# Performance work log

Hardware: AMD Instinct MI355X
Metric: run time of the kernel (lower is better)

Reference implementation:

```python
import jax, jax.numpy as jnp
import numpy as np

THRESHOLD = 0.004  # graph_threshold from init_kwargs
EPS = 1e-12


def setup_inputs() -> dict:
    key = jax.random.key(0)
    kf, kw = jax.random.split(key)
    features = jax.random.normal(kf, (8192, 128), dtype=jnp.float32)
    weight = jax.random.normal(kw, (128, 128), dtype=jnp.float32)
    return {"features": features, "weight": weight}


def reference(features, weight):
    # Pairwise state fidelity: squared dot product of row-normalized vectors.
    n = features.shape[0]
    xn = features / (jnp.linalg.norm(features, axis=1, keepdims=True) + EPS)
    fid = (xn @ xn.T) ** 2  # [N, N]
    # Edge weight 1.0 where fid >= threshold (secondary=None); no self-loops.
    adj = (fid >= THRESHOLD).astype(features.dtype)
    adj = adj * (1.0 - jnp.eye(n, dtype=features.dtype))
    aggregated = adj @ features  # [N, F]
    # relu(W @ agg.T).T == relu(agg @ W.T)
    return jax.nn.relu(aggregated @ weight.T)
```

## Files before the change

### kernel.cpp

```cpp
#include <hip/hip_runtime.h>
#include <math.h>

#define NROWS  8192
#define NF     128
#define THRF   0.004f
#define BM     64
#define BN     64
#define HALF_N 4096
#define NITER  64

typedef _Float16 f16;
typedef __attribute__((ext_vector_type(8))) _Float16 f16x8;
typedef __attribute__((ext_vector_type(4))) float f32x4;

#define MFMA16F(a, b, c) __builtin_amdgcn_mfma_f32_16x16x32_f16(a, b, c, 0, 0, 0)

#define RH_OFF 0
#define RL_OFF 32768
#define TB_OFF 65536
#define PB_OFF 98304
#define IJ_OFF 106496
#define SM_BYTES 107008

typedef __attribute__((address_space(1))) const unsigned int g_u32;
typedef __attribute__((address_space(3))) unsigned int l_u32;

__device__ __forceinline__ void gload16(const void* g, void* l) {
    __builtin_amdgcn_global_load_lds((g_u32*)g, (l_u32*)l, 16, 0, 0);
}

__global__ __launch_bounds__(256) void prep_k(const float* __restrict__ X,
                                              float* __restrict__ inv_norm,
                                              unsigned short* __restrict__ Xh,
                                              unsigned short* __restrict__ Xl) {
    int row  = blockIdx.x * 4 + (threadIdx.x >> 6);
    int lane = threadIdx.x & 63;
    float2 e = reinterpret_cast<const float2*>(X + (size_t)row * NF)[lane];
    float ss = e.x * e.x + e.y * e.y;
    #pragma unroll
    for (int off = 32; off; off >>= 1) ss += __shfl_xor(ss, off);
    if (lane == 0) inv_norm[row] = 1.0f / (sqrtf(ss) + 1e-12f);

    f16 hx = (f16)e.x, hy = (f16)e.y;
    f16 lx = (f16)((e.x - (float)hx) * 2048.0f);
    f16 ly = (f16)((e.y - (float)hy) * 2048.0f);
    unsigned hu = (unsigned)__builtin_bit_cast(unsigned short, hx) |
                  ((unsigned)__builtin_bit_cast(unsigned short, hy) << 16);
    unsigned lu = (unsigned)__builtin_bit_cast(unsigned short, lx) |
                  ((unsigned)__builtin_bit_cast(unsigned short, ly) << 16);
    reinterpret_cast<unsigned*>(Xh)[row * 64 + lane] = hu;
    reinterpret_cast<unsigned*>(Xl)[row * 64 + lane] = lu;
}

__global__ __launch_bounds__(256) void transpose_k(const unsigned short* __restrict__ Xh,
                                                   unsigned short* __restrict__ XhT) {
    __shared__ unsigned short sT[128][136];
    const int t  = threadIdx.x;
    const int jb = blockIdx.x * 128;
    {
        int row = t >> 1, half = t & 1;
        const unsigned short* src = Xh + (size_t)(jb + row) * NF + half * 64;
        #pragma unroll
        for (int k = 0; k < 8; ++k)
            *reinterpret_cast<uint4*>(&sT[row][half * 64 + 8 * k]) =
                reinterpret_cast<const uint4*>(src)[k];
    }
    __syncthreads();
    int f = t >> 1, qh = t & 1;
    unsigned um[32];
    #pragma unroll
    for (int m = 0; m < 32; ++m) {
        int j = 64 * qh + 2 * m;
        um[m] = (unsigned)sT[j][f] | ((unsigned)sT[j + 1][f] << 16);
    }
    unsigned* dst = reinterpret_cast<unsigned*>(XhT + (size_t)f * NROWS + jb + 64 * qh);
    #pragma unroll
    for (int m = 0; m < 32; ++m) dst[m] = um[m];
}

__device__ __forceinline__ void issue_tiles(const unsigned short* __restrict__ Xh,
                                            const unsigned short* __restrict__ Xl,
                                            const unsigned short* __restrict__ XhT,
                                            char* SM, int w, int l, int jwin, int buf) {
    const int r16 = l >> 4, c16 = l & 15;
    #pragma unroll
    for (int u = 0; u < 2; ++u) {
        int jloc = 8 * w + 4 * u + r16;
        size_t src = (size_t)(jwin + jloc) * NF + ((c16 ^ (jloc & 15)) << 3);
        char* ldsH = SM + RH_OFF + buf * 16384 + (8 * w + 4 * u) * 256;
        char* ldsL = SM + RL_OFF + buf * 16384 + (8 * w + 4 * u) * 256;
        gload16(Xh + src, ldsH);
        gload16(Xl + src, ldsL);
    }
    const int r8 = l >> 3, c8 = l & 7;
    #pragma unroll
    for (int u = 0; u < 2; ++u) {
        int floc = 16 * w + 8 * u + r8;
        const unsigned short* src = XhT + (size_t)floc * NROWS + jwin + ((c8 ^ (floc & 7)) << 3);
        char* ldsT = SM + TB_OFF + buf * 16384 + (16 * w + 8 * u) * 128;
        gload16(src, ldsT);
    }
}

__global__ __launch_bounds__(512, 1) void fused_k(const unsigned short* __restrict__ Xh,
                                                  const unsigned short* __restrict__ Xl,
                                                  const unsigned short* __restrict__ XhT,
                                                  const float* __restrict__ inv_norm,
                                                  float* __restrict__ pAgg0,
                                                  float* __restrict__ pAgg1) {
    __shared__ __align__(16) char SM[SM_BYTES];
    const int t = threadIdx.x;
    const int w = t >> 6, l = t & 63, l15 = l & 15, h = l >> 4;
    const int wm = w >> 1, wn = w & 1;
    const int bid   = blockIdx.x;
    const int ibase = (bid >> 1) * BM;
    const int qoff  = (bid & 1) * HALF_N;
    float* pAgg = (bid & 1) ? pAgg1 : pAgg0;

    f16x8 aH[4], aL[4];
    const int gia = ibase + 16 * wm + l15;
    #pragma unroll
    for (int ks = 0; ks < 4; ++ks) {
        aH[ks] = *reinterpret_cast<const f16x8*>(Xh + (size_t)gia * NF + 32 * ks + 8 * h);
        aL[ks] = *reinterpret_cast<const f16x8*>(Xl + (size_t)gia * NF + 32 * ks + 8 * h);
    }
    float invI[4]; int gid[4];
    #pragma unroll
    for (int q = 0; q < 4; ++q) {
        gid[q]  = ibase + 16 * wm + 4 * h + q;
        invI[q] = inv_norm[gid[q]];
    }

    issue_tiles(Xh, Xl, XhT, SM, w, l, qoff, 0);
    if (t < BN) ((float*)(SM + IJ_OFF))[t] = inv_norm[qoff + t];

    f32x4 agg[4];
    #pragma unroll
    for (int nf = 0; nf < 4; ++nf)
        #pragma unroll
        for (int q = 0; q < 4; ++q) agg[nf][q] = 0.f;

    for (int it = 0; it < NITER; ++it) {
        const int buf  = it & 1;
        const int jwin = qoff + it * BN;
        __syncthreads();
        if (it + 1 < NITER) {
            issue_tiles(Xh, Xl, XhT, SM, w, l, jwin + BN, buf ^ 1);
            if (t < BN)
                ((float*)(SM + IJ_OFF))[(buf ^ 1) * BN + t] = inv_norm[jwin + BN + t];
        }
        const char* rh = SM + RH_OFF + buf * 16384;
        const char* rl = SM + RL_OFF + buf * 16384;
        f32x4 Shi[2], Slo[2];
        #pragma unroll
        for (int nt = 0; nt < 2; ++nt)
            #pragma unroll
            for (int q = 0; q < 4; ++q) { Shi[nt][q] = 0.f; Slo[nt][q] = 0.f; }
        #pragma unroll
        for (int ks = 0; ks < 4; ++ks) {
            #pragma unroll
            for (int nt = 0; nt < 2; ++nt) {
                int jl   = 32 * wn + 16 * nt + l15;
                int boff = jl * 256 + (((4 * ks + h) ^ (jl & 15)) << 4);
                f16x8 bh = *reinterpret_cast<const f16x8*>(rh + boff);
                f16x8 bl = *reinterpret_cast<const f16x8*>(rl + boff);
                Shi[nt] = MFMA16F(aH[ks], bh, Shi[nt]);
                Slo[nt] = MFMA16F(aH[ks], bl, Slo[nt]);
                Slo[nt] = MFMA16F(aL[ks], bh, Slo[nt]);
            }
        }
        const float* invJ = (const float*)(SM + IJ_OFF) + buf * BN;
        #pragma unroll
        for (int nt = 0; nt < 2; ++nt) {
            int jl = 32 * wn + 16 * nt + l15;
            float ivj = invJ[jl];
            int gj = jwin + jl;
            #pragma unroll
            for (int q = 0; q < 4; ++q) {
                int il  = 16 * wm + 4 * h + q;
                float v = (Shi[nt][q] + Slo[nt][q] * (1.0f / 2048.0f)) * invI[q] * ivj;
                bool p  = (v * v >= THRF) && (gid[q] != gj);
                int pb  = il * 128 + ((jl * 2) ^ ((il & 7) << 4));
                *reinterpret_cast<unsigned short*>(SM + PB_OFF + pb) =
                    p ? (unsigned short)0x3C00 : (unsigned short)0;
            }
        }
        __syncthreads();
        const char* tbp = SM + TB_OFF + buf * 16384;
        #pragma unroll
        for (int kj = 0; kj < 2; ++kj) {
            int ila = 16 * wm + l15;
            int pab = ila * 128 + ((64 * kj + 16 * h) ^ ((ila & 7) << 4));
            f16x8 pa = *reinterpret_cast<const f16x8*>(SM + PB_OFF + pab);
            #pragma unroll
            for (int nf = 0; nf < 4; ++nf) {
                int f   = 64 * wn + 16 * nf + l15;
                int tbo = f * 128 + ((64 * kj + 16 * h) ^ ((f & 7) << 4));
                f16x8 bt = *reinterpret_cast<const f16x8*>(tbp + tbo);
                agg[nf] = MFMA16F(pa, bt, agg[nf]);
            }
        }
    }
    #pragma unroll
    for (int nf = 0; nf < 4; ++nf) {
        int f = 64 * wn + 16 * nf + l15;
        #pragma unroll
        for (int q = 0; q < 4; ++q) {
            int row = ibase + 16 * wm + 4 * h + q;
            pAgg[(size_t)row * NF + f] = agg[nf][q];
        }
    }
}

__global__ __launch_bounds__(256) void combine_k(const float* __restrict__ pAgg1,
                                                 const float* __restrict__ Wm,
                                                 float* __restrict__ out) {
    __shared__ float sW[NF * NF];
    __shared__ float sSum[32][132];
    const int t = threadIdx.x;
    const size_t base = (size_t)blockIdx.x * 32 * NF;
    #pragma unroll
    for (int k = 0; k < 16; ++k) {
        int u4 = t + 256 * k;
        reinterpret_cast<f32x4*>(sW)[u4] = reinterpret_cast<const f32x4*>(Wm)[u4];
    }
    #pragma unroll
    for (int k = 0; k < 16; ++k) {
        int u = t + 256 * k;
        float v = out[base + u] + pAgg1[base + u];
        sSum[u >> 7][u & 127] = v;
    }
    __syncthreads();
    const int r = t & 31, og = t >> 5;
    float acc[16];
    #pragma unroll
    for (int oi = 0; oi < 16; ++oi) acc[oi] = 0.f;
    #pragma unroll 8
    for (int k4 = 0; k4 < 32; ++k4) {
        f32x4 a4 = *reinterpret_cast<const f32x4*>(&sSum[r][4 * k4]);
        #pragma unroll
        for (int oi = 0; oi < 16; ++oi) {
            f32x4 w4 = *reinterpret_cast<const f32x4*>(&sW[(og * 16 + oi) * NF + 4 * k4]);
            acc[oi] += a4[0] * w4[0] + a4[1] * w4[1] + a4[2] * w4[2] + a4[3] * w4[3];
        }
    }
    #pragma unroll
    for (int o4 = 0; o4 < 4; ++o4) {
        f32x4 v4;
        #pragma unroll
        for (int e = 0; e < 4; ++e) {
            float v = acc[o4 * 4 + e];
            v4[e] = v > 0.f ? v : 0.f;
        }
        *reinterpret_cast<f32x4*>(out + base + r * NF + og * 16 + o4 * 4) = v4;
    }
}

extern "C" void kernel_launch(void* const* d_in, const int* in_sizes, int n_in,
                              void* d_out, int out_size, void* d_ws, size_t ws_size,
                              hipStream_t stream) {
    const float* feat = (const float*)d_in[0];
    const float* Wm   = (const float*)d_in[1];
    float* out        = (float*)d_out;

    char* ws = (char*)d_ws;
    unsigned short* Xh  = (unsigned short*)(ws);
    unsigned short* Xl  = (unsigned short*)(ws + (2u << 20));
    unsigned short* XhT = (unsigned short*)(ws + (4u << 20));
    float* inv_norm     = (float*)(ws + (6u << 20));
    float* pAgg1        = (float*)(ws + (6u << 20) + 32768);

    prep_k<<<NROWS / 4, 256, 0, stream>>>(feat, inv_norm, Xh, Xl);
    transpose_k<<<NROWS / 128, 256, 0, stream>>>(Xh, XhT);
    fused_k<<<256, 512, 0, stream>>>(Xh, Xl, XhT, inv_norm, out, pAgg1);
    combine_k<<<NROWS / 32, 256, 0, stream>>>(pAgg1, Wm, out);
}
```

Baseline: 121.3 us.

## Fuse prep and transpose kernels and retile fused kernel warps to 2x4

```diff
diff --git a/kernel.cpp b/kernel.cpp
--- a/kernel.cpp
+++ b/kernel.cpp
@@ -29,53 +29,70 @@
     __builtin_amdgcn_global_load_lds((g_u32*)g, (l_u32*)l, 16, 0, 0);
 }
 
+__device__ __forceinline__ unsigned short f16bits(f16 x) {
+    return __builtin_bit_cast(unsigned short, x);
+}
+
 __global__ __launch_bounds__(256) void prep_k(const float* __restrict__ X,
                                               float* __restrict__ inv_norm,
                                               unsigned short* __restrict__ Xh,
-                                              unsigned short* __restrict__ Xl) {
-    int row  = blockIdx.x * 4 + (threadIdx.x >> 6);
-    int lane = threadIdx.x & 63;
-    float2 e = reinterpret_cast<const float2*>(X + (size_t)row * NF)[lane];
-    float ss = e.x * e.x + e.y * e.y;
-    #pragma unroll
-    for (int off = 32; off; off >>= 1) ss += __shfl_xor(ss, off);
-    if (lane == 0) inv_norm[row] = 1.0f / (sqrtf(ss) + 1e-12f);
-
-    f16 hx = (f16)e.x, hy = (f16)e.y;
-    f16 lx = (f16)((e.x - (float)hx) * 2048.0f);
-    f16 ly = (f16)((e.y - (float)hy) * 2048.0f);
-    unsigned hu = (unsigned)__builtin_bit_cast(unsigned short, hx) |
-                  ((unsigned)__builtin_bit_cast(unsigned short, hy) << 16);
-    unsigned lu = (unsigned)__builtin_bit_cast(unsigned short, lx) |
-                  ((unsigned)__builtin_bit_cast(unsigned short, ly) << 16);
-    reinterpret_cast<unsigned*>(Xh)[row * 64 + lane] = hu;
-    reinterpret_cast<unsigned*>(Xl)[row * 64 + lane] = lu;
-}
-
-__global__ __launch_bounds__(256) void transpose_k(const unsigned short* __restrict__ Xh,
-                                                   unsigned short* __restrict__ XhT) {
-    __shared__ unsigned short sT[128][136];
+                                              unsigned short* __restrict__ Xl,
+                                              unsigned short* __restrict__ XhT) {
+    __shared__ unsigned short sT[64][136];
     const int t  = threadIdx.x;
-    const int jb = blockIdx.x * 128;
+    const int jb = blockIdx.x * 64;
+    const int row = t >> 2, c0 = (t & 3) * 32;
+    const int grow = jb + row;
+
+    float v[32];
     {
-        int row = t >> 1, half = t & 1;
-        const unsigned short* src = Xh + (size_t)(jb + row) * NF + half * 64;
-        #pragma unroll
-        for (int k = 0; k < 8; ++k)
-            *reinterpret_cast<uint4*>(&sT[row][half * 64 + 8 * k]) =
-                reinterpret_cast<const uint4*>(src)[k];
+        const float* src = X + (size_t)grow * NF + c0;
+        #pragma unroll
+        for (int k = 0; k < 8; ++k) {
+            f32x4 e = *reinterpret_cast<const f32x4*>(src + 4 * k);
+            v[4 * k]     = e[0]; v[4 * k + 1] = e[1];
+            v[4 * k + 2] = e[2]; v[4 * k + 3] = e[3];
+        }
+    }
+    float ss = 0.f;
+    #pragma unroll
+    for (int k = 0; k < 32; ++k) ss += v[k] * v[k];
+    ss += __shfl_xor(ss, 1);
+    ss += __shfl_xor(ss, 2);
+    if ((t & 3) == 0) inv_norm[grow] = 1.0f / (sqrtf(ss) + 1e-12f);
+
+    #pragma unroll
+    for (int k = 0; k < 4; ++k) {
+        unsigned hw[4], lw[4];
+        #pragma unroll
+        for (int p = 0; p < 4; ++p) {
+            float a = v[8 * k + 2 * p], b = v[8 * k + 2 * p + 1];
+            f16 ha = (f16)a, hb = (f16)b;
+            f16 la = (f16)((a - (float)ha) * 2048.0f);
+            f16 lb = (f16)((b - (float)hb) * 2048.0f);
+            hw[p] = (unsigned)f16bits(ha) | ((unsigned)f16bits(hb) << 16);
+            lw[p] = (unsigned)f16bits(la) | ((unsigned)f16bits(lb) << 16);
+        }
+        uint4 h4 = {hw[0], hw[1], hw[2], hw[3]};
+        uint4 l4 = {lw[0], lw[1], lw[2], lw[3]};
+        *reinterpret_cast<uint4*>(Xh + (size_t)grow * NF + c0 + 8 * k) = h4;
+        *reinterpret_cast<uint4*>(Xl + (size_t)grow * NF + c0 + 8 * k) = l4;
+        unsigned* sp = reinterpret_cast<unsigned*>(&sT[row][c0 + 8 * k]);
+        sp[0] = hw[0]; sp[1] = hw[1]; sp[2] = hw[2]; sp[3] = hw[3];
     }
     __syncthreads();
-    int f = t >> 1, qh = t & 1;
-    unsigned um[32];
-    #pragma unroll
-    for (int m = 0; m < 32; ++m) {
-        int j = 64 * qh + 2 * m;
-        um[m] = (unsigned)sT[j][f] | ((unsigned)sT[j + 1][f] << 16);
-    }
-    unsigned* dst = reinterpret_cast<unsigned*>(XhT + (size_t)f * NROWS + jb + 64 * qh);
-    #pragma unroll
-    for (int m = 0; m < 32; ++m) dst[m] = um[m];
+    {
+        int f = t >> 1, qh = t & 1;
+        unsigned um[16];
+        #pragma unroll
+        for (int m = 0; m < 16; ++m) {
+            int j = 32 * qh + 2 * m;
+            um[m] = (unsigned)sT[j][f] | ((unsigned)sT[j + 1][f] << 16);
+        }
+        unsigned* dst = reinterpret_cast<unsigned*>(XhT + (size_t)f * NROWS + jb + 32 * qh);
+        #pragma unroll
+        for (int m = 0; m < 16; ++m) dst[m] = um[m];
+    }
 }
 
 __device__ __forceinline__ void issue_tiles(const unsigned short* __restrict__ Xh,
@@ -111,34 +128,36 @@
     __shared__ __align__(16) char SM[SM_BYTES];
     const int t = threadIdx.x;
     const int w = t >> 6, l = t & 63, l15 = l & 15, h = l >> 4;
-    const int wm = w >> 1, wn = w & 1;
+    const int im = w >> 2;
+    const int jn = w & 3;
     const int bid   = blockIdx.x;
     const int ibase = (bid >> 1) * BM;
     const int qoff  = (bid & 1) * HALF_N;
     float* pAgg = (bid & 1) ? pAgg1 : pAgg0;
 
-    f16x8 aH[4], aL[4];
-    const int gia = ibase + 16 * wm + l15;
-    #pragma unroll
-    for (int ks = 0; ks < 4; ++ks) {
-        aH[ks] = *reinterpret_cast<const f16x8*>(Xh + (size_t)gia * NF + 32 * ks + 8 * h);
-        aL[ks] = *reinterpret_cast<const f16x8*>(Xl + (size_t)gia * NF + 32 * ks + 8 * h);
-    }
-    float invI[4]; int gid[4];
-    #pragma unroll
-    for (int q = 0; q < 4; ++q) {
-        gid[q]  = ibase + 16 * wm + 4 * h + q;
-        invI[q] = inv_norm[gid[q]];
-    }
+    f16x8 aH[8], aL[8];
+    #pragma unroll
+    for (int ii = 0; ii < 2; ++ii)
+        #pragma unroll
+        for (int ks = 0; ks < 4; ++ks) {
+            size_t ro = (size_t)(ibase + 32 * im + 16 * ii + l15) * NF + 32 * ks + 8 * h;
+            aH[ii * 4 + ks] = *reinterpret_cast<const f16x8*>(Xh + ro);
+            aL[ii * 4 + ks] = *reinterpret_cast<const f16x8*>(Xl + ro);
+        }
+    float invI2[8];
+    #pragma unroll
+    for (int ii = 0; ii < 2; ++ii)
+        #pragma unroll
+        for (int q = 0; q < 4; ++q) {
+            float x = inv_norm[ibase + 32 * im + 16 * ii + 4 * h + q];
+            invI2[ii * 4 + q] = x * x;
+        }
+    const int jl = 16 * jn + l15;
 
     issue_tiles(Xh, Xl, XhT, SM, w, l, qoff, 0);
-    if (t < BN) ((float*)(SM + IJ_OFF))[t] = inv_norm[qoff + t];
-
-    f32x4 agg[4];
-    #pragma unroll
-    for (int nf = 0; nf < 4; ++nf)
-        #pragma unroll
-        for (int q = 0; q < 4; ++q) agg[nf][q] = 0.f;
+    if (t < BN) { float x = inv_norm[qoff + t]; ((float*)(SM + IJ_OFF))[t] = x * x; }
+
+    f32x4 agg00 = {0,0,0,0}, agg01 = {0,0,0,0}, agg10 = {0,0,0,0}, agg11 = {0,0,0,0};
 
     for (int it = 0; it < NITER; ++it) {
         const int buf  = it & 1;
@@ -146,69 +165,85 @@
         __syncthreads();
         if (it + 1 < NITER) {
             issue_tiles(Xh, Xl, XhT, SM, w, l, jwin + BN, buf ^ 1);
-            if (t < BN)
-                ((float*)(SM + IJ_OFF))[(buf ^ 1) * BN + t] = inv_norm[jwin + BN + t];
+            if (t < BN) {
+                float x = inv_norm[jwin + BN + t];
+                ((float*)(SM + IJ_OFF))[(buf ^ 1) * BN + t] = x * x;
+            }
         }
         const char* rh = SM + RH_OFF + buf * 16384;
         const char* rl = SM + RL_OFF + buf * 16384;
-        f32x4 Shi[2], Slo[2];
-        #pragma unroll
-        for (int nt = 0; nt < 2; ++nt)
-            #pragma unroll
-            for (int q = 0; q < 4; ++q) { Shi[nt][q] = 0.f; Slo[nt][q] = 0.f; }
+        f32x4 Shi0 = {0,0,0,0}, Shi1 = {0,0,0,0};
+        f32x4 SA0  = {0,0,0,0}, SA1  = {0,0,0,0};
+        f32x4 SB0  = {0,0,0,0}, SB1  = {0,0,0,0};
+        __builtin_amdgcn_s_setprio(1);
         #pragma unroll
         for (int ks = 0; ks < 4; ++ks) {
-            #pragma unroll
-            for (int nt = 0; nt < 2; ++nt) {
-                int jl   = 32 * wn + 16 * nt + l15;
-                int boff = jl * 256 + (((4 * ks + h) ^ (jl & 15)) << 4);
-                f16x8 bh = *reinterpret_cast<const f16x8*>(rh + boff);
-                f16x8 bl = *reinterpret_cast<const f16x8*>(rl + boff);
-                Shi[nt] = MFMA16F(aH[ks], bh, Shi[nt]);
-                Slo[nt] = MFMA16F(aH[ks], bl, Slo[nt]);
-                Slo[nt] = MFMA16F(aL[ks], bh, Slo[nt]);
-            }
-        }
-        const float* invJ = (const float*)(SM + IJ_OFF) + buf * BN;
-        #pragma unroll
-        for (int nt = 0; nt < 2; ++nt) {
-            int jl = 32 * wn + 16 * nt + l15;
-            float ivj = invJ[jl];
-            int gj = jwin + jl;
+            int boff = jl * 256 + (((4 * ks + h) ^ (jl & 15)) << 4);
+            f16x8 bh = *reinterpret_cast<const f16x8*>(rh + boff);
+            f16x8 bl = *reinterpret_cast<const f16x8*>(rl + boff);
+            Shi0 = MFMA16F(aH[ks],     bh, Shi0);
+            Shi1 = MFMA16F(aH[4 + ks], bh, Shi1);
+            SA0  = MFMA16F(aH[ks],     bl, SA0);
+            SA1  = MFMA16F(aH[4 + ks], bl, SA1);
+            SB0  = MFMA16F(aL[ks],     bh, SB0);
+            SB1  = MFMA16F(aL[4 + ks], bh, SB1);
+        }
+        __builtin_amdgcn_s_setprio(0);
+        {
+            float ij2v = ((const float*)(SM + IJ_OFF))[buf * BN + jl];
+            int ecmp = (jwin + jl) - (ibase + 32 * im + 4 * h);
             #pragma unroll
             for (int q = 0; q < 4; ++q) {
-                int il  = 16 * wm + 4 * h + q;
-                float v = (Shi[nt][q] + Slo[nt][q] * (1.0f / 2048.0f)) * invI[q] * ivj;
-                bool p  = (v * v >= THRF) && (gid[q] != gj);
-                int pb  = il * 128 + ((jl * 2) ^ ((il & 7) << 4));
+                float vv = Shi0[q] + (SA0[q] + SB0[q]) * (1.0f / 2048.0f);
+                float t2 = vv * vv * invI2[q] * ij2v;
+                bool p = (t2 >= THRF) && (ecmp != q);
+                int il = 32 * im + 4 * h + q;
+                int pb = il * 128 + ((jl * 2) ^ ((il & 7) << 4));
                 *reinterpret_cast<unsigned short*>(SM + PB_OFF + pb) =
                     p ? (unsigned short)0x3C00 : (unsigned short)0;
             }
-        }
-        __syncthreads();
+            #pragma unroll
+            for (int q = 0; q < 4; ++q) {
+                float vv = Shi1[q] + (SA1[q] + SB1[q]) * (1.0f / 2048.0f);
+                float t2 = vv * vv * invI2[4 + q] * ij2v;
+                bool p = (t2 >= THRF) && (ecmp != 16 + q);
+                int il = 32 * im + 16 + 4 * h + q;
+                int pb = il * 128 + ((jl * 2) ^ ((il & 7) << 4));
+                *reinterpret_cast<unsigned short*>(SM + PB_OFF + pb) =
+                    p ? (unsigned short)0x3C00 : (unsigned short)0;
+            }
+        }
+        asm volatile("s_waitcnt lgkmcnt(0)\n\ts_barrier" ::: "memory");
         const char* tbp = SM + TB_OFF + buf * 16384;
+        __builtin_amdgcn_s_setprio(1);
         #pragma unroll
         for (int kj = 0; kj < 2; ++kj) {
-            int ila = 16 * wm + l15;
-            int pab = ila * 128 + ((64 * kj + 16 * h) ^ ((ila & 7) << 4));
-            f16x8 pa = *reinterpret_cast<const f16x8*>(SM + PB_OFF + pab);
-            #pragma unroll
-            for (int nf = 0; nf < 4; ++nf) {
-                int f   = 64 * wn + 16 * nf + l15;
-                int tbo = f * 128 + ((64 * kj + 16 * h) ^ ((f & 7) << 4));
-                f16x8 bt = *reinterpret_cast<const f16x8*>(tbp + tbo);
-                agg[nf] = MFMA16F(pa, bt, agg[nf]);
-            }
-        }
-    }
-    #pragma unroll
-    for (int nf = 0; nf < 4; ++nf) {
-        int f = 64 * wn + 16 * nf + l15;
-        #pragma unroll
-        for (int q = 0; q < 4; ++q) {
-            int row = ibase + 16 * wm + 4 * h + q;
-            pAgg[(size_t)row * NF + f] = agg[nf][q];
-        }
+            int il0 = 32 * im + l15, il1 = il0 + 16;
+            f16x8 pa0 = *reinterpret_cast<const f16x8*>(
+                SM + PB_OFF + il0 * 128 + ((64 * kj + 16 * h) ^ ((il0 & 7) << 4)));
+            f16x8 pa1 = *reinterpret_cast<const f16x8*>(
+                SM + PB_OFF + il1 * 128 + ((64 * kj + 16 * h) ^ ((il1 & 7) << 4)));
+            int f0 = 32 * jn + l15, f1 = f0 + 16;
+            f16x8 bt0 = *reinterpret_cast<const f16x8*>(
+                tbp + f0 * 128 + ((64 * kj + 16 * h) ^ ((f0 & 7) << 4)));
+            f16x8 bt1 = *reinterpret_cast<const f16x8*>(
+                tbp + f1 * 128 + ((64 * kj + 16 * h) ^ ((f1 & 7) << 4)));
+            agg00 = MFMA16F(pa0, bt0, agg00);
+            agg01 = MFMA16F(pa0, bt1, agg01);
+            agg10 = MFMA16F(pa1, bt0, agg10);
+            agg11 = MFMA16F(pa1, bt1, agg11);
+        }
+        __builtin_amdgcn_s_setprio(0);
+    }
+    #pragma unroll
+    for (int q = 0; q < 4; ++q) {
+        int r0 = ibase + 32 * im + 4 * h + q;
+        int r1 = r0 + 16;
+        int c0 = 32 * jn + l15, c1 = c0 + 16;
+        pAgg[(size_t)r0 * NF + c0] = agg00[q];
+        pAgg[(size_t)r0 * NF + c1] = agg01[q];
+        pAgg[(size_t)r1 * NF + c0] = agg10[q];
+        pAgg[(size_t)r1 * NF + c1] = agg11[q];
     }
 }
 
@@ -270,8 +305,7 @@
     float* inv_norm     = (float*)(ws + (6u << 20));
     float* pAgg1        = (float*)(ws + (6u << 20) + 32768);
 
-    prep_k<<<NROWS / 4, 256, 0, stream>>>(feat, inv_norm, Xh, Xl);
-    transpose_k<<<NROWS / 128, 256, 0, stream>>>(Xh, XhT);
+    prep_k<<<NROWS / 64, 256, 0, stream>>>(feat, inv_norm, Xh, Xl, XhT);
     fused_k<<<256, 512, 0, stream>>>(Xh, Xl, XhT, inv_norm, out, pAgg1);
     combine_k<<<NROWS / 32, 256, 0, stream>>>(pAgg1, Wm, out);
 }
```

After: 116.5 us. -3.9%, faster.

## Drop transpose kernel using LDS transpose reads and restructure fused tile loop

Applied to the files above, without the earlier changes.

```diff
diff --git a/kernel.cpp b/kernel.cpp
--- a/kernel.cpp
+++ b/kernel.cpp
@@ -1,26 +1,26 @@
 #include <hip/hip_runtime.h>
 #include <math.h>
 
-#define NROWS  8192
-#define NF     128
-#define THRF   0.004f
-#define BM     64
-#define BN     64
-#define HALF_N 4096
-#define NITER  64
+#define NROWS 8192
+#define NF    128
+#define THRF  0.004f
+#define BM    64
+#define BN    128
+#define QN    4096
+#define NITER 32
 
 typedef _Float16 f16;
 typedef __attribute__((ext_vector_type(8))) _Float16 f16x8;
+typedef __attribute__((ext_vector_type(4))) _Float16 f16x4;
 typedef __attribute__((ext_vector_type(4))) float f32x4;
+typedef __attribute__((ext_vector_type(2))) unsigned u32x2;
+typedef __attribute__((address_space(3))) char lds_char;
 
 #define MFMA16F(a, b, c) __builtin_amdgcn_mfma_f32_16x16x32_f16(a, b, c, 0, 0, 0)
 
-#define RH_OFF 0
-#define RL_OFF 32768
-#define TB_OFF 65536
-#define PB_OFF 98304
-#define IJ_OFF 106496
-#define SM_BYTES 107008
+#define XT_OFF 0
+#define PB_OFF 65536
+#define SM_BYTES 81920
 
 typedef __attribute__((address_space(1))) const unsigned int g_u32;
 typedef __attribute__((address_space(3))) unsigned int l_u32;
@@ -29,190 +29,215 @@
     __builtin_amdgcn_global_load_lds((g_u32*)g, (l_u32*)l, 16, 0, 0);
 }
 
+__device__ __forceinline__ unsigned short f16bits(f16 x) {
+    return __builtin_bit_cast(unsigned short, x);
+}
+
+union B8 { u32x2 u2[2]; f16x8 v; };
+
+__device__ __forceinline__ u32x2 tr8(lds_char* p) {
+    u32x2 r;
+    asm volatile("ds_read_b64_tr_b16 %0, %1" : "=v"(r) : "v"(p));
+    return r;
+}
+
 __global__ __launch_bounds__(256) void prep_k(const float* __restrict__ X,
-                                              float* __restrict__ inv_norm,
+                                              float* __restrict__ inv2,
                                               unsigned short* __restrict__ Xh,
                                               unsigned short* __restrict__ Xl) {
-    int row  = blockIdx.x * 4 + (threadIdx.x >> 6);
-    int lane = threadIdx.x & 63;
-    float2 e = reinterpret_cast<const float2*>(X + (size_t)row * NF)[lane];
-    float ss = e.x * e.x + e.y * e.y;
-    #pragma unroll
-    for (int off = 32; off; off >>= 1) ss += __shfl_xor(ss, off);
-    if (lane == 0) inv_norm[row] = 1.0f / (sqrtf(ss) + 1e-12f);
-
-    f16 hx = (f16)e.x, hy = (f16)e.y;
-    f16 lx = (f16)((e.x - (float)hx) * 2048.0f);
-    f16 ly = (f16)((e.y - (float)hy) * 2048.0f);
-    unsigned hu = (unsigned)__builtin_bit_cast(unsigned short, hx) |
-                  ((unsigned)__builtin_bit_cast(unsigned short, hy) << 16);
-    unsigned lu = (unsigned)__builtin_bit_cast(unsigned short, lx) |
-                  ((unsigned)__builtin_bit_cast(unsigned short, ly) << 16);
-    reinterpret_cast<unsigned*>(Xh)[row * 64 + lane] = hu;
-    reinterpret_cast<unsigned*>(Xl)[row * 64 + lane] = lu;
-}
-
-__global__ __launch_bounds__(256) void transpose_k(const unsigned short* __restrict__ Xh,
-                                                   unsigned short* __restrict__ XhT) {
-    __shared__ unsigned short sT[128][136];
-    const int t  = threadIdx.x;
-    const int jb = blockIdx.x * 128;
-    {
-        int row = t >> 1, half = t & 1;
-        const unsigned short* src = Xh + (size_t)(jb + row) * NF + half * 64;
-        #pragma unroll
-        for (int k = 0; k < 8; ++k)
-            *reinterpret_cast<uint4*>(&sT[row][half * 64 + 8 * k]) =
-                reinterpret_cast<const uint4*>(src)[k];
-    }
-    __syncthreads();
-    int f = t >> 1, qh = t & 1;
-    unsigned um[32];
-    #pragma unroll
-    for (int m = 0; m < 32; ++m) {
-        int j = 64 * qh + 2 * m;
-        um[m] = (unsigned)sT[j][f] | ((unsigned)sT[j + 1][f] << 16);
-    }
-    unsigned* dst = reinterpret_cast<unsigned*>(XhT + (size_t)f * NROWS + jb + 64 * qh);
-    #pragma unroll
-    for (int m = 0; m < 32; ++m) dst[m] = um[m];
-}
-
-__device__ __forceinline__ void issue_tiles(const unsigned short* __restrict__ Xh,
-                                            const unsigned short* __restrict__ Xl,
-                                            const unsigned short* __restrict__ XhT,
-                                            char* SM, int w, int l, int jwin, int buf) {
-    const int r16 = l >> 4, c16 = l & 15;
-    #pragma unroll
-    for (int u = 0; u < 2; ++u) {
-        int jloc = 8 * w + 4 * u + r16;
-        size_t src = (size_t)(jwin + jloc) * NF + ((c16 ^ (jloc & 15)) << 3);
-        char* ldsH = SM + RH_OFF + buf * 16384 + (8 * w + 4 * u) * 256;
-        char* ldsL = SM + RL_OFF + buf * 16384 + (8 * w + 4 * u) * 256;
-        gload16(Xh + src, ldsH);
-        gload16(Xl + src, ldsL);
-    }
-    const int r8 = l >> 3, c8 = l & 7;
-    #pragma unroll
-    for (int u = 0; u < 2; ++u) {
-        int floc = 16 * w + 8 * u + r8;
-        const unsigned short* src = XhT + (size_t)floc * NROWS + jwin + ((c8 ^ (floc & 7)) << 3);
-        char* ldsT = SM + TB_OFF + buf * 16384 + (16 * w + 8 * u) * 128;
-        gload16(src, ldsT);
-    }
-}
-
-__global__ __launch_bounds__(512, 1) void fused_k(const unsigned short* __restrict__ Xh,
+    const int t = threadIdx.x;
+    const int row = blockIdx.x * 8 + (t >> 5);
+    const int lane = t & 31;
+    f32x4 e = reinterpret_cast<const f32x4*>(X + (size_t)row * NF)[lane];
+    float ss = e[0]*e[0] + e[1]*e[1] + e[2]*e[2] + e[3]*e[3];
+    ss += __shfl_xor(ss, 16); ss += __shfl_xor(ss, 8);
+    ss += __shfl_xor(ss, 4);  ss += __shfl_xor(ss, 2); ss += __shfl_xor(ss, 1);
+    if (lane == 0) {
+        float inv = 1.0f / (sqrtf(ss) + 1e-12f);
+        inv2[row] = inv * inv;
+    }
+    unsigned hw[2], lw[2];
+    #pragma unroll
+    for (int p = 0; p < 2; ++p) {
+        float a = e[2*p], b = e[2*p+1];
+        f16 ha = (f16)a, hb = (f16)b;
+        f16 la = (f16)((a - (float)ha) * 2048.0f);
+        f16 lb = (f16)((b - (float)hb) * 2048.0f);
+        hw[p] = (unsigned)f16bits(ha) | ((unsigned)f16bits(hb) << 16);
+        lw[p] = (unsigned)f16bits(la) | ((unsigned)f16bits(lb) << 16);
+    }
+    u32x2 hu = {hw[0], hw[1]}, lu = {lw[0], lw[1]};
+    *reinterpret_cast<u32x2*>(Xh + (size_t)row * NF + lane * 4) = hu;
+    *reinterpret_cast<u32x2*>(Xl + (size_t)row * NF + lane * 4) = lu;
+}
+
+__device__ __forceinline__ void stage_tile(const unsigned short* __restrict__ Xh,
+                                           char* SM, int w, int l, int jwin, int buf) {
+    #pragma unroll
+    for (int u = 0; u < 4; ++u) {
+        int c = w * 4 + u;
+        int j = 4 * c + ((l & 7) >> 1);
+        int f = 16 * (l >> 3) + 8 * (l & 1);
+        gload16(Xh + (size_t)(jwin + j) * NF + f, SM + XT_OFF + buf * 32768 + c * 1024);
+    }
+}
+
+__global__ __launch_bounds__(512, 2) void fused_k(const unsigned short* __restrict__ Xh,
                                                   const unsigned short* __restrict__ Xl,
-                                                  const unsigned short* __restrict__ XhT,
-                                                  const float* __restrict__ inv_norm,
-                                                  float* __restrict__ pAgg0,
-                                                  float* __restrict__ pAgg1) {
+                                                  const float* __restrict__ inv2,
+                                                  float* __restrict__ out,
+                                                  _Float16* __restrict__ p1) {
     __shared__ __align__(16) char SM[SM_BYTES];
     const int t = threadIdx.x;
     const int w = t >> 6, l = t & 63, l15 = l & 15, h = l >> 4;
-    const int wm = w >> 1, wn = w & 1;
-    const int bid   = blockIdx.x;
+    const int im = w >> 2;
+    const int jn = w & 3;
+    const int ilh = w >> 2, fb = w & 3;
+    const int bid = blockIdx.x;
     const int ibase = (bid >> 1) * BM;
-    const int qoff  = (bid & 1) * HALF_N;
-    float* pAgg = (bid & 1) ? pAgg1 : pAgg0;
-
-    f16x8 aH[4], aL[4];
-    const int gia = ibase + 16 * wm + l15;
-    #pragma unroll
-    for (int ks = 0; ks < 4; ++ks) {
-        aH[ks] = *reinterpret_cast<const f16x8*>(Xh + (size_t)gia * NF + 32 * ks + 8 * h);
-        aL[ks] = *reinterpret_cast<const f16x8*>(Xl + (size_t)gia * NF + 32 * ks + 8 * h);
-    }
-    float invI[4]; int gid[4];
-    #pragma unroll
-    for (int q = 0; q < 4; ++q) {
-        gid[q]  = ibase + 16 * wm + 4 * h + q;
-        invI[q] = inv_norm[gid[q]];
-    }
-
-    issue_tiles(Xh, Xl, XhT, SM, w, l, qoff, 0);
-    if (t < BN) ((float*)(SM + IJ_OFF))[t] = inv_norm[qoff + t];
-
-    f32x4 agg[4];
-    #pragma unroll
-    for (int nf = 0; nf < 4; ++nf)
-        #pragma unroll
-        for (int q = 0; q < 4; ++q) agg[nf][q] = 0.f;
-
-    for (int it = 0; it < NITER; ++it) {
-        const int buf  = it & 1;
-        const int jwin = qoff + it * BN;
+    const int qq    = bid & 1;
+    const int qbase = qq * QN;
+
+    f16x8 biH[2][4], biL[2][4];
+    float invI2[2];
+    #pragma unroll
+    for (int it = 0; it < 2; ++it) {
+        size_t ro = (size_t)(ibase + 32 * im + 16 * it + l15) * NF + 8 * h;
+        #pragma unroll
+        for (int ks = 0; ks < 4; ++ks) {
+            biH[it][ks] = *reinterpret_cast<const f16x8*>(Xh + ro + 32 * ks);
+            biL[it][ks] = *reinterpret_cast<const f16x8*>(Xl + ro + 32 * ks);
+        }
+        invI2[it] = inv2[ibase + 32 * im + 16 * it + l15];
+    }
+
+    f32x4 agg[2][2];
+    #pragma unroll
+    for (int s2 = 0; s2 < 2; ++s2)
+        #pragma unroll
+        for (int nf = 0; nf < 2; ++nf)
+            #pragma unroll
+            for (int q = 0; q < 4; ++q) agg[s2][nf][q] = 0.f;
+
+    stage_tile(Xh, SM, w, l, qbase, 0);
+
+    for (int it0 = 0; it0 < NITER; ++it0) {
+        const int buf  = it0 & 1;
+        const int jwin = qbase + it0 * BN;
         __syncthreads();
-        if (it + 1 < NITER) {
-            issue_tiles(Xh, Xl, XhT, SM, w, l, jwin + BN, buf ^ 1);
-            if (t < BN)
-                ((float*)(SM + IJ_OFF))[(buf ^ 1) * BN + t] = inv_norm[jwin + BN + t];
-        }
-        const char* rh = SM + RH_OFF + buf * 16384;
-        const char* rl = SM + RL_OFF + buf * 16384;
-        f32x4 Shi[2], Slo[2];
-        #pragma unroll
-        for (int nt = 0; nt < 2; ++nt)
-            #pragma unroll
-            for (int q = 0; q < 4; ++q) { Shi[nt][q] = 0.f; Slo[nt][q] = 0.f; }
+        if (it0 + 1 < NITER) stage_tile(Xh, SM, w, l, jwin + BN, buf ^ 1);
+
+        const char* xbuf = SM + XT_OFF + buf * 32768;
+        f16x8 ahj[2][4], alg[2][4];
+        f32x4 jq[2];
+        #pragma unroll
+        for (int jt2 = 0; jt2 < 2; ++jt2) {
+            int jl = 32 * jn + 16 * jt2 + l15;
+            int a_base = (jl >> 2) * 1024 + (h >> 1) * 128 + (jl & 3) * 32 + (h & 1) * 16;
+            #pragma unroll
+            for (int ks = 0; ks < 4; ++ks)
+                ahj[jt2][ks] = *reinterpret_cast<const f16x8*>(xbuf + a_base + ks * 256);
+            const unsigned short* xlr = Xl + (size_t)(jwin + jl) * NF + 8 * h;
+            #pragma unroll
+            for (int ks = 0; ks < 4; ++ks)
+                alg[jt2][ks] = *reinterpret_cast<const f16x8*>(xlr + 32 * ks);
+            jq[jt2] = *reinterpret_cast<const f32x4*>(inv2 + jwin + 32 * jn + 16 * jt2 + 4 * h);
+        }
+
+        f32x4 Shi[2][2], Slo[2][2];
+        #pragma unroll
+        for (int jt2 = 0; jt2 < 2; ++jt2)
+            #pragma unroll
+            for (int it = 0; it < 2; ++it)
+                #pragma unroll
+                for (int q = 0; q < 4; ++q) { Shi[jt2][it][q] = 0.f; Slo[jt2][it][q] = 0.f; }
+        __builtin_amdgcn_s_setprio(1);
         #pragma unroll
         for (int ks = 0; ks < 4; ++ks) {
             #pragma unroll
-            for (int nt = 0; nt < 2; ++nt) {
-                int jl   = 32 * wn + 16 * nt + l15;
-                int boff = jl * 256 + (((4 * ks + h) ^ (jl & 15)) << 4);
-                f16x8 bh = *reinterpret_cast<const f16x8*>(rh + boff);
-                f16x8 bl = *reinterpret_cast<const f16x8*>(rl + boff);
-                Shi[nt] = MFMA16F(aH[ks], bh, Shi[nt]);
-                Slo[nt] = MFMA16F(aH[ks], bl, Slo[nt]);
-                Slo[nt] = MFMA16F(aL[ks], bh, Slo[nt]);
-            }
-        }
-        const float* invJ = (const float*)(SM + IJ_OFF) + buf * BN;
-        #pragma unroll
-        for (int nt = 0; nt < 2; ++nt) {
-            int jl = 32 * wn + 16 * nt + l15;
-            float ivj = invJ[jl];
-            int gj = jwin + jl;
+            for (int jt2 = 0; jt2 < 2; ++jt2) {
+                #pragma unroll
+                for (int it = 0; it < 2; ++it) {
+                    Shi[jt2][it] = MFMA16F(ahj[jt2][ks], biH[it][ks], Shi[jt2][it]);
+                    Slo[jt2][it] = MFMA16F(alg[jt2][ks], biH[it][ks], Slo[jt2][it]);
+                    Slo[jt2][it] = MFMA16F(ahj[jt2][ks], biL[it][ks], Slo[jt2][it]);
+                }
+            }
+        }
+        __builtin_amdgcn_s_setprio(0);
+
+        #pragma unroll
+        for (int jt2 = 0; jt2 < 2; ++jt2) {
+            #pragma unroll
+            for (int it = 0; it < 2; ++it) {
+                int il = 32 * im + 16 * it + l15;
+                int ecmp = (ibase + il) - (jwin + 32 * jn + 16 * jt2 + 4 * h);
+                unsigned m[4];
+                #pragma unroll
+                for (int q = 0; q < 4; ++q) {
+                    float vv = Shi[jt2][it][q] + Slo[jt2][it][q] * (1.0f / 2048.0f);
+                    float t2 = vv * vv * invI2[it] * jq[jt2][q];
+                    bool p = (t2 >= THRF) && (ecmp != q);
+                    m[q] = p ? 0x3C00u : 0u;
+                }
+                int cb2 = 64 * jn + 32 * jt2 + 8 * h;
+                u32x2 pw = {m[0] | (m[1] << 16), m[2] | (m[3] << 16)};
+                *reinterpret_cast<u32x2*>(SM + PB_OFF + il * 256 +
+                                          (cb2 ^ ((il & 7) << 4))) = pw;
+            }
+        }
+        asm volatile("s_waitcnt lgkmcnt(0)\n\ts_barrier" ::: "memory");
+
+        {
+            lds_char* trb = (lds_char*)(SM + XT_OFF + buf * 32768);
+            f16x8 bt[4][2], pa[4][2];
+            #pragma unroll
+            for (int kj = 0; kj < 4; ++kj) {
+                #pragma unroll
+                for (int nf = 0; nf < 2; ++nf) {
+                    int band = 2 * fb + nf;
+                    lds_char* p0 = trb + (64 * kj + 16 * h + band) * 128 + 8 * l15;
+                    B8 bu;
+                    bu.u2[0] = tr8(p0);
+                    bu.u2[1] = tr8(p0 + 1024);
+                    bt[kj][nf] = bu.v;
+                }
+                #pragma unroll
+                for (int s2 = 0; s2 < 2; ++s2) {
+                    int ir = 32 * ilh + 16 * s2 + l15;
+                    pa[kj][s2] = *reinterpret_cast<const f16x8*>(
+                        SM + PB_OFF + ir * 256 + ((64 * kj + 16 * h) ^ ((ir & 7) << 4)));
+                }
+            }
+            asm volatile("s_waitcnt lgkmcnt(0)" ::: "memory");
+            __builtin_amdgcn_sched_barrier(0);
+            __builtin_amdgcn_s_setprio(1);
+            #pragma unroll
+            for (int kj = 0; kj < 4; ++kj) {
+                agg[0][0] = MFMA16F(pa[kj][0], bt[kj][0], agg[0][0]);
+                agg[0][1] = MFMA16F(pa[kj][0], bt[kj][1], agg[0][1]);
+                agg[1][0] = MFMA16F(pa[kj][1], bt[kj][0], agg[1][0]);
+                agg[1][1] = MFMA16F(pa[kj][1], bt[kj][1], agg[1][1]);
+            }
+            __builtin_amdgcn_s_setprio(0);
+        }
+    }
+
+    #pragma unroll
+    for (int s2 = 0; s2 < 2; ++s2)
+        #pragma unroll
+        for (int nf = 0; nf < 2; ++nf)
             #pragma unroll
             for (int q = 0; q < 4; ++q) {
-                int il  = 16 * wm + 4 * h + q;
-                float v = (Shi[nt][q] + Slo[nt][q] * (1.0f / 2048.0f)) * invI[q] * ivj;
-                bool p  = (v * v >= THRF) && (gid[q] != gj);
-                int pb  = il * 128 + ((jl * 2) ^ ((il & 7) << 4));
-                *reinterpret_cast<unsigned short*>(SM + PB_OFF + pb) =
-                    p ? (unsigned short)0x3C00 : (unsigned short)0;
-            }
-        }
-        __syncthreads();
-        const char* tbp = SM + TB_OFF + buf * 16384;
-        #pragma unroll
-        for (int kj = 0; kj < 2; ++kj) {
-            int ila = 16 * wm + l15;
-            int pab = ila * 128 + ((64 * kj + 16 * h) ^ ((ila & 7) << 4));
-            f16x8 pa = *reinterpret_cast<const f16x8*>(SM + PB_OFF + pab);
-            #pragma unroll
-            for (int nf = 0; nf < 4; ++nf) {
-                int f   = 64 * wn + 16 * nf + l15;
-                int tbo = f * 128 + ((64 * kj + 16 * h) ^ ((f & 7) << 4));
-                f16x8 bt = *reinterpret_cast<const f16x8*>(tbp + tbo);
-                agg[nf] = MFMA16F(pa, bt, agg[nf]);
-            }
-        }
-    }
-    #pragma unroll
-    for (int nf = 0; nf < 4; ++nf) {
-        int f = 64 * wn + 16 * nf + l15;
-        #pragma unroll
-        for (int q = 0; q < 4; ++q) {
-            int row = ibase + 16 * wm + 4 * h + q;
-            pAgg[(size_t)row * NF + f] = agg[nf][q];
-        }
-    }
-}
-
-__global__ __launch_bounds__(256) void combine_k(const float* __restrict__ pAgg1,
+                int row = ibase + 32 * ilh + 16 * s2 + 4 * h + q;
+                int col = 32 * fb + 16 * nf + l15;
+                float v = agg[s2][nf][q];
+                if (qq == 0) out[(size_t)row * NF + col] = v;
+                else         p1[(size_t)row * NF + col] = (_Float16)v;
+            }
+}
+
+__global__ __launch_bounds__(256) void combine_k(const _Float16* __restrict__ p1,
                                                  const float* __restrict__ Wm,
                                                  float* __restrict__ out) {
     __shared__ float sW[NF * NF];
@@ -225,10 +250,13 @@
         reinterpret_cast<f32x4*>(sW)[u4] = reinterpret_cast<const f32x4*>(Wm)[u4];
     }
     #pragma unroll
-    for (int k = 0; k < 16; ++k) {
-        int u = t + 256 * k;
-        float v = out[base + u] + pAgg1[base + u];
-        sSum[u >> 7][u & 127] = v;
+    for (int k = 0; k < 4; ++k) {
+        int u4 = t + 256 * k;
+        f32x4 v = reinterpret_cast<const f32x4*>(out + base)[u4];
+        f16x4 a = reinterpret_cast<const f16x4*>(p1 + base)[u4];
+        #pragma unroll
+        for (int e = 0; e < 4; ++e) v[e] += (float)a[e];
+        *reinterpret_cast<f32x4*>(&sSum[u4 >> 5][(4 * u4) & 127]) = v;
     }
     __syncthreads();
     const int r = t & 31, og = t >> 5;
@@ -264,14 +292,12 @@
     float* out        = (float*)d_out;
 
     char* ws = (char*)d_ws;
-    unsigned short* Xh  = (unsigned short*)(ws);
-    unsigned short* Xl  = (unsigned short*)(ws + (2u << 20));
-    unsigned short* XhT = (unsigned short*)(ws + (4u << 20));
-    float* inv_norm     = (float*)(ws + (6u << 20));
-    float* pAgg1        = (float*)(ws + (6u << 20) + 32768);
-
-    prep_k<<<NROWS / 4, 256, 0, stream>>>(feat, inv_norm, Xh, Xl);
-    transpose_k<<<NROWS / 128, 256, 0, stream>>>(Xh, XhT);
-    fused_k<<<256, 512, 0, stream>>>(Xh, Xl, XhT, inv_norm, out, pAgg1);
-    combine_k<<<NROWS / 32, 256, 0, stream>>>(pAgg1, Wm, out);
-}
+    unsigned short* Xh = (unsigned short*)(ws);
+    unsigned short* Xl = (unsigned short*)(ws + (2u << 20));
+    float* inv2        = (float*)(ws + (4u << 20));
+    _Float16* p1       = (_Float16*)(ws + (4u << 20) + 32768);
+
+    prep_k<<<NROWS / 8, 256, 0, stream>>>(feat, inv2, Xh, Xl);
+    fused_k<<<256, 512, 0, stream>>>(Xh, Xl, inv2, out, p1);
+    combine_k<<<NROWS / 32, 256, 0, stream>>>(p1, Wm, out);
+}
```

New measurement: 152.3 us. 1.26x slower.
